# Kernel tuning notes

Hardware: AMD Instinct MI355X
Metric: run time of the kernel (lower is better)

Reference implementation:

```python
import jax, jax.numpy as jnp
import numpy as np

D_MODEL = 2048
HEADS = 16
K = D_MODEL // HEADS  # 128
FFN = 8192


def rms_norm(x):
    # mean of squares over last dim, no eps (matches source)
    ms = jnp.mean(jnp.square(x), axis=2, keepdims=True)
    return x / jnp.sqrt(ms)


def setup_inputs() -> dict:
    key = jax.random.key(0)
    ks = jax.random.split(key, 9)
    s = D_MODEL ** (-0.5)
    B, S = 2, 2048
    return {
        "x_BSE": jax.random.normal(ks[0], (B, S, D_MODEL), jnp.float32),
        "w_q": jax.random.normal(ks[1], (D_MODEL, HEADS, K), jnp.float32) * s,
        "w_k": jax.random.normal(ks[2], (D_MODEL, HEADS, K), jnp.float32) * s,
        "w_v": jax.random.normal(ks[3], (D_MODEL, HEADS, K), jnp.float32) * s,
        "w_o": jax.random.normal(ks[4], (D_MODEL, HEADS, K), jnp.float32) * s,
        "w1": jax.random.normal(ks[5], (D_MODEL, FFN), jnp.float32) * s,
        "b1": jax.random.normal(ks[6], (1, FFN), jnp.float32) * s,
        "w2": jax.random.normal(ks[7], (FFN, D_MODEL), jnp.float32) * s,
        "b2": jax.random.normal(ks[8], (1, D_MODEL), jnp.float32) * s,
    }


def attention(x, w_q, w_k, w_v, w_o):
    q = jnp.einsum('bse,ehk->bshk', x, w_q)
    k = jnp.einsum('bme,ehk->bmhk', x, w_k)
    v = jnp.einsum('bme,ehk->bmhk', x, w_v)
    logits = jnp.einsum('bshk,bmhk->bshm', q, k) / jnp.sqrt(jnp.float32(K))
    S = x.shape[1]
    causal = jnp.arange(S)[:, None] >= jnp.arange(S)[None, :]  # [S, M]
    logits = jnp.where(causal[None, :, None, :], logits, -jnp.inf)
    probs = jax.nn.softmax(logits, axis=3)
    out = jnp.einsum('bshm,bmhk->bshk', probs, v)
    return jnp.einsum('bshk,ehk->bse', out, w_o)


def ffn(x, w1, b1, w2, b2):
    h = jnp.clip(x @ w1 + b1, 0.0, 6.0)  # ReLU6
    return h @ w2 + b2


def reference(x_BSE, w_q, w_k, w_v, w_o, w1, b1, w2, b2):
    x = x_BSE + attention(rms_norm(x_BSE), w_q, w_k, w_v, w_o)
    x = x + ffn(rms_norm(x), w1, b1, w2, b2)
    return x
```

## Files before the change

### kernel.cpp

```cpp
#include <hip/hip_runtime.h>
#include <hip/hip_bf16.h>
#include <stdint.h>

typedef __attribute__((ext_vector_type(8))) short bf16x8;
typedef __attribute__((ext_vector_type(4))) float f32x4;
typedef unsigned short ushort_t;

typedef __attribute__((address_space(1))) char as1_char;
typedef __attribute__((address_space(3))) char as3_char;

__device__ __forceinline__ void gload_lds16(const void* g, void* l) {
  __builtin_amdgcn_global_load_lds((as1_char*)g, (as3_char*)l, 16, 0, 0);
}

template <int N> __device__ __forceinline__ void waitvm() {
  asm volatile("s_waitcnt vmcnt(%0)" :: "n"(N) : "memory");
}

__device__ __forceinline__ unsigned short f2bf(float f) {
  union { float f; unsigned u; } c; c.f = f;
  unsigned u = c.u;
  return (unsigned short)((u + 0x7fffu + ((u >> 16) & 1u)) >> 16);
}

__global__ __launch_bounds__(256)
void rmsnorm_kernel(const float* __restrict__ x, unsigned short* __restrict__ out) {
  const int tok = blockIdx.x;
  const int tid = threadIdx.x;
  const float4* xr = (const float4*)(x + (size_t)tok * 2048);
  float4 a = xr[tid];
  float4 b = xr[tid + 256];
  float s = a.x*a.x + a.y*a.y + a.z*a.z + a.w*a.w
          + b.x*b.x + b.y*b.y + b.z*b.z + b.w*b.w;
  #pragma unroll
  for (int m = 1; m < 64; m <<= 1) s += __shfl_xor(s, m);
  __shared__ float ws4[4];
  if ((tid & 63) == 0) ws4[tid >> 6] = s;
  __syncthreads();
  const float tot = ws4[0] + ws4[1] + ws4[2] + ws4[3];
  const float r = rsqrtf(tot * (1.0f / 2048.0f));
  ushort4 o1, o2;
  o1.x = f2bf(a.x * r); o1.y = f2bf(a.y * r); o1.z = f2bf(a.z * r); o1.w = f2bf(a.w * r);
  o2.x = f2bf(b.x * r); o2.y = f2bf(b.y * r); o2.z = f2bf(b.z * r); o2.w = f2bf(b.w * r);
  ushort4* orow = (ushort4*)(out + (size_t)tok * 2048);
  orow[tid] = o1;
  orow[tid + 256] = o2;
}

__global__ __launch_bounds__(256)
void transpose_cvt(const float* __restrict__ in, unsigned short* __restrict__ out,
                   int R, int C) {
  __shared__ float t[32][33];
  const int c0 = blockIdx.x * 32, r0 = blockIdx.y * 32;
  const int tx = threadIdx.x, ty = threadIdx.y;
  #pragma unroll
  for (int i = 0; i < 4; i++)
    t[ty + 8 * i][tx] = in[(size_t)(r0 + ty + 8 * i) * C + (c0 + tx)];
  __syncthreads();
  #pragma unroll
  for (int i = 0; i < 4; i++)
    out[(size_t)(c0 + ty + 8 * i) * R + (r0 + tx)] = f2bf(t[tx][ty + 8 * i]);
}

__global__ __launch_bounds__(256)
void cvt_bf16_kernel(const float* __restrict__ in, unsigned short* __restrict__ out, int n4) {
  const int i = blockIdx.x * 256 + threadIdx.x;
  if (i < n4) {
    float4 v = ((const float4*)in)[i];
    ushort4 o; o.x = f2bf(v.x); o.y = f2bf(v.y); o.z = f2bf(v.z); o.w = f2bf(v.w);
    ((ushort4*)out)[i] = o;
  }
}

template <int BN, int EPI>
__global__ __launch_bounds__(512, 2)
void gemm256(const ushort_t* __restrict__ A, const ushort_t* __restrict__ B,
             int K, int N,
             ushort_t* ob0, ushort_t* ob1, ushort_t* ob2, float* outf,
             const float* __restrict__ res, const float* __restrict__ bias,
             int nbx) {
  constexpr int LB = (BN * 64) / 8192;
  constexpr int LPT = 2 + LB;
  constexpr int NR = BN / 64;
  constexpr int WN = BN / 4;
  constexpr int BUFSZ = 16384 + BN * 64;
  __shared__ __align__(16) char smem[4 * BUFSZ];

  const int tid = threadIdx.x;
  const int lane = tid & 63;
  const int wid = tid >> 6;
  const int wm = wid >> 2, wn = wid & 3;
  const int ln15 = lane & 15, g = lane >> 4;

  int wg = blockIdx.x;
  const int cpx = gridDim.x >> 3;
  wg = (wg & 7) * cpx + (wg >> 3);
  const int bx = wg % nbx, by = wg / nbx;
  const int m0 = by * 256, n0 = bx * BN;

  const char* Ab = (const char*)(A + (size_t)m0 * K);
  const char* Bb = (const char*)(B + (size_t)n0 * K);
  const size_t rowb = (size_t)K * 2;
  const int NT = K >> 5;

  auto stage = [&](int t, int s) {
    char* As = smem + s * BUFSZ;
    char* Bs = As + 16384;
    const size_t kb = (size_t)t * 64;
    #pragma unroll
    for (int i = 0; i < 2; i++) {
      const int o = i * 8192 + tid * 16;
      const int row = o >> 6, col = o & 63;
      gload_lds16(Ab + (size_t)row * rowb + kb + (col ^ ((row & 3) << 4)), As + o);
    }
    #pragma unroll
    for (int i = 0; i < LB; i++) {
      const int o = i * 8192 + tid * 16;
      const int row = o >> 6, col = o & 63;
      gload_lds16(Bb + (size_t)row * rowb + kb + (col ^ ((row & 3) << 4)), Bs + o);
    }
  };

  f32x4 acc[8][NR] = {};

  stage(0, 0); stage(1, 1); stage(2, 2);

  for (int t = 0; t < NT; ++t) {
    if (t + 3 < NT) {
      stage(t + 3, (t + 3) & 3);
      waitvm<3 * LPT>();
    } else {
      const int rem = NT - 1 - t;
      if (rem >= 2)      waitvm<2 * LPT>();
      else if (rem == 1) waitvm<LPT>();
      else               waitvm<0>();
    }
    __builtin_amdgcn_s_barrier();

    const char* As = smem + (t & 3) * BUFSZ;
    const char* Bs = As + 16384;

    bf16x8 af[8], bfm[NR];
    #pragma unroll
    for (int mi = 0; mi < 8; mi++) {
      const int row = wm * 128 + mi * 16 + ln15;
      af[mi] = *(const bf16x8*)(As + row * 64 + ((g * 16) ^ ((row & 3) << 4)));
    }
    #pragma unroll
    for (int ni = 0; ni < NR; ni++) {
      const int row = wn * WN + ni * 16 + ln15;
      bfm[ni] = *(const bf16x8*)(Bs + row * 64 + ((g * 16) ^ ((row & 3) << 4)));
    }
    asm volatile("" ::: "memory");
    __builtin_amdgcn_s_barrier();

    __builtin_amdgcn_s_setprio(1);
    #pragma unroll
    for (int mi = 0; mi < 8; mi++)
      #pragma unroll
      for (int ni = 0; ni < NR; ni++)
        acc[mi][ni] = __builtin_amdgcn_mfma_f32_16x16x32_bf16(af[mi], bfm[ni], acc[mi][ni], 0, 0, 0);
    __builtin_amdgcn_s_setprio(0);
  }

  #pragma unroll
  for (int mi = 0; mi < 8; mi++) {
    const int mrow = m0 + wm * 128 + mi * 16 + g * 4;
    #pragma unroll
    for (int ni = 0; ni < NR; ni++) {
      const int ncol = n0 + wn * WN + ni * 16 + ln15;
      if (EPI == 0) {
        const int region = n0 >> 11;
        if (region == 0) {
          #pragma unroll
          for (int r = 0; r < 4; r++)
            ob0[(size_t)(mrow + r) * 2048 + ncol] = f2bf(acc[mi][ni][r]);
        } else if (region == 1) {
          #pragma unroll
          for (int r = 0; r < 4; r++)
            ob1[(size_t)(mrow + r) * 2048 + (ncol - 2048)] = f2bf(acc[mi][ni][r]);
        } else {
          const int bb = mrow >> 11, ss = mrow & 2047;
          const int ncv = ncol - 4096;
          const int hh = ncv >> 7, dd = ncv & 127;
          ushort4 v;
          v.x = f2bf(acc[mi][ni][0]); v.y = f2bf(acc[mi][ni][1]);
          v.z = f2bf(acc[mi][ni][2]); v.w = f2bf(acc[mi][ni][3]);
          *(ushort4*)(ob2 + ((size_t)((bb * 16 + hh) * 128 + dd)) * 2048 + ss) = v;
        }
      } else if (EPI == 2) {
        const float bv = bias[ncol];
        #pragma unroll
        for (int r = 0; r < 4; r++) {
          float v = acc[mi][ni][r] + bv;
          v = fminf(fmaxf(v, 0.0f), 6.0f);
          ob0[(size_t)(mrow + r) * N + ncol] = f2bf(v);
        }
      } else {
        const float bv = bias ? bias[ncol] : 0.0f;
        #pragma unroll
        for (int r = 0; r < 4; r++) {
          const size_t idx = (size_t)(mrow + r) * N + ncol;
          outf[idx] = res[idx] + acc[mi][ni][r] + bv;
        }
      }
    }
  }
}

__global__ __launch_bounds__(256)
void attn_kernel(const unsigned short* __restrict__ Qg,
                 const unsigned short* __restrict__ Kg,
                 const unsigned short* __restrict__ Vg,
                 unsigned short* __restrict__ Og) {
  __shared__ __align__(16) char smem[65536];
  const int tid = threadIdx.x, lane = tid & 63, wid = tid >> 6;
  const int g = lane >> 4, qq = lane & 15;
  const int pairx = blockIdx.x, h = blockIdx.y, b = blockIdx.z;

  auto stage = [&](int kv0, char* kdst, char* vdst) {
    #pragma unroll
    for (int i = 0; i < 4; i++) {
      const int oo = i * 4096 + tid * 16;
      const int rK = oo >> 8;
      const int sK = (oo & 255) ^ ((rK & 7) << 4);
      gload_lds16((const char*)Kg + ((size_t)(b * 2048 + kv0 + rK) * 2048 + h * 128) * 2 + sK,
                  kdst + oo);
      const int rV = oo >> 7;
      const int sV = (oo & 127) ^ ((rV & 7) << 4);
      gload_lds16((const char*)Vg + ((size_t)((b * 16 + h) * 128 + rV) * 2048 + kv0) * 2 + sV,
                  vdst + oo);
    }
  };

  for (int half = 0; half < 2; ++half) {
    const int qb = half ? (31 - pairx) : pairx;
    const int q0 = qb * 64;
    const int myq = q0 + wid * 16 + qq;
    const int nt = qb + 1;

    bf16x8 qf[4];
    const unsigned short* qp = Qg + ((size_t)(b * 2048 + myq)) * 2048 + h * 128 + g * 8;
    #pragma unroll
    for (int ks = 0; ks < 4; ks++) qf[ks] = *(const bf16x8*)(qp + ks * 32);

    stage(0, smem, smem + 16384);

    float m_run = -1e30f, l_run = 0.0f;
    f32x4 oacc[8] = {};

    for (int t = 0; t < nt; ++t) {
      const int cur = t & 1;
      char* kbc = cur ? smem + 32768 : smem;
      char* vbc = cur ? smem + 49152 : smem + 16384;
      char* kbn = cur ? smem : smem + 32768;
      char* vbn = cur ? smem + 16384 : smem + 49152;

      if (t + 1 < nt) {
        stage((t + 1) * 64, kbn, vbn);
        asm volatile("s_waitcnt vmcnt(8)" ::: "memory");
      } else {
        asm volatile("s_waitcnt vmcnt(0)" ::: "memory");
      }
      __builtin_amdgcn_s_barrier();
      asm volatile("" ::: "memory");

      const int kv0 = t * 64;

      f32x4 st[4] = {};
      __builtin_amdgcn_s_setprio(1);
      #pragma unroll
      for (int ks = 0; ks < 4; ks++) {
        #pragma unroll
        for (int f = 0; f < 4; f++) {
          const int row = f * 16 + qq;
          const int cb = ks * 64 + g * 16;
          bf16x8 kf = *(const bf16x8*)(kbc + row * 256 + (cb ^ ((row & 7) << 4)));
          st[f] = __builtin_amdgcn_mfma_f32_16x16x32_bf16(kf, qf[ks], st[f], 0, 0, 0);
        }
      }
      __builtin_amdgcn_s_setprio(0);

      float p[4][4];
      float tmax = -3.0e38f;
      const bool diag = (t == qb);
      #pragma unroll
      for (int f = 0; f < 4; f++) {
        #pragma unroll
        for (int r = 0; r < 4; r++) {
          float v = st[f][r] * 0.08838834764831845f;
          if (diag) {
            const int kv = kv0 + f * 16 + g * 4 + r;
            if (kv > myq) v = -3.0e38f;
          }
          p[f][r] = v;
          tmax = fmaxf(tmax, v);
        }
      }
      tmax = fmaxf(tmax, __shfl_xor(tmax, 16));
      tmax = fmaxf(tmax, __shfl_xor(tmax, 32));
      const float m_new = fmaxf(m_run, tmax);
      const float sf = __expf(m_run - m_new);
      m_run = m_new;
      float tsum = 0.0f;
      #pragma unroll
      for (int f = 0; f < 4; f++) {
        #pragma unroll
        for (int r = 0; r < 4; r++) {
          p[f][r] = __expf(p[f][r] - m_new);
          tsum += p[f][r];
        }
      }
      tsum += __shfl_xor(tsum, 16);
      tsum += __shfl_xor(tsum, 32);
      l_run = l_run * sf + tsum;

      unsigned pk[4][2];
      #pragma unroll
      for (int f = 0; f < 4; f++) {
        pk[f][0] = (unsigned)f2bf(p[f][0]) | ((unsigned)f2bf(p[f][1]) << 16);
        pk[f][1] = (unsigned)f2bf(p[f][2]) | ((unsigned)f2bf(p[f][3]) << 16);
      }
      bf16x8 pa[2];
      const int sel = g >> 1;
      #pragma unroll
      for (int ks2 = 0; ks2 < 2; ks2++) {
        unsigned d[4];
        #pragma unroll
        for (int u = 0; u < 2; u++) {
          const int sl = qq + (((2 * g + u) & 3) << 4);
          const unsigned lo0 = (unsigned)__shfl((int)pk[2 * ks2][0], sl);
          const unsigned hi0 = (unsigned)__shfl((int)pk[2 * ks2 + 1][0], sl);
          const unsigned lo1 = (unsigned)__shfl((int)pk[2 * ks2][1], sl);
          const unsigned hi1 = (unsigned)__shfl((int)pk[2 * ks2 + 1][1], sl);
          d[2 * u]     = sel ? hi0 : lo0;
          d[2 * u + 1] = sel ? hi1 : lo1;
        }
        union { unsigned u[4]; bf16x8 v; } cv;
        cv.u[0] = d[0]; cv.u[1] = d[1]; cv.u[2] = d[2]; cv.u[3] = d[3];
        pa[ks2] = cv.v;
      }

      float sfr[4];
      #pragma unroll
      for (int r = 0; r < 4; r++) sfr[r] = __shfl(sf, g * 4 + r);
      #pragma unroll
      for (int nf = 0; nf < 8; nf++) {
        oacc[nf][0] *= sfr[0]; oacc[nf][1] *= sfr[1];
        oacc[nf][2] *= sfr[2]; oacc[nf][3] *= sfr[3];
      }
      __builtin_amdgcn_s_setprio(1);
      #pragma unroll
      for (int nf = 0; nf < 8; nf++) {
        #pragma unroll
        for (int ks2 = 0; ks2 < 2; ks2++) {
          const int row = nf * 16 + qq;
          const int cb = ks2 * 64 + g * 16;
          bf16x8 vf = *(const bf16x8*)(vbc + row * 128 + (cb ^ ((row & 7) << 4)));
          oacc[nf] = __builtin_amdgcn_mfma_f32_16x16x32_bf16(pa[ks2], vf, oacc[nf], 0, 0, 0);
        }
      }
      __builtin_amdgcn_s_setprio(0);

      asm volatile("" ::: "memory");
      __builtin_amdgcn_s_barrier();
    }

    asm volatile("" ::: "memory");
    const float inv = 1.0f / l_run;
    float invr[4];
    #pragma unroll
    for (int r = 0; r < 4; r++) invr[r] = __shfl(inv, g * 4 + r);

    float* Osm = (float*)smem;
    #pragma unroll
    for (int nf = 0; nf < 8; nf++) {
      #pragma unroll
      for (int r = 0; r < 4; r++)
        Osm[(wid * 16 + g * 4 + r) * 132 + nf * 16 + qq] = oacc[nf][r] * invr[r];
    }
    __syncthreads();
    #pragma unroll
    for (int it = 0; it < 4; it++) {
      const int row = it * 16 + (tid >> 4);
      const int c0 = (tid & 15) * 8;
      const float* src = &Osm[row * 132 + c0];
      uint4 w;
      w.x = (unsigned)f2bf(src[0]) | ((unsigned)f2bf(src[1]) << 16);
      w.y = (unsigned)f2bf(src[2]) | ((unsigned)f2bf(src[3]) << 16);
      w.z = (unsigned)f2bf(src[4]) | ((unsigned)f2bf(src[5]) << 16);
      w.w = (unsigned)f2bf(src[6]) | ((unsigned)f2bf(src[7]) << 16);
      *(uint4*)(Og + (size_t)(b * 2048 + q0 + row) * 2048 + h * 128 + c0) = w;
    }
    __syncthreads();
  }
}

extern "C" void kernel_launch(void* const* d_in, const int* in_sizes, int n_in,
                              void* d_out, int out_size, void* d_ws, size_t ws_size,
                              hipStream_t stream) {
  (void)in_sizes; (void)n_in; (void)out_size; (void)ws_size;
  const float* x  = (const float*)d_in[0];
  const float* wq = (const float*)d_in[1];
  const float* wk = (const float*)d_in[2];
  const float* wv = (const float*)d_in[3];
  const float* wo = (const float*)d_in[4];
  const float* w1 = (const float*)d_in[5];
  const float* b1 = (const float*)d_in[6];
  const float* w2 = (const float*)d_in[7];
  const float* b2 = (const float*)d_in[8];
  float* out = (float*)d_out;
  char* ws = (char*)d_ws;

  ushort_t* wqkvT = (ushort_t*)(ws + 0);
  ushort_t* wqT = wqkvT;
  ushort_t* wkT = (ushort_t*)(ws + 8388608);
  ushort_t* wvT = (ushort_t*)(ws + 16777216);
  ushort_t* woC = (ushort_t*)(ws + 25165824);
  ushort_t* w1T = (ushort_t*)(ws + 33554432);
  ushort_t* w2T = (ushort_t*)(ws + 67108864);
  ushort_t* h1  = (ushort_t*)(ws + 100663296);
  ushort_t* Qb  = (ushort_t*)(ws + 117440512);
  ushort_t* Kb  = (ushort_t*)(ws + 134217728);
  ushort_t* Vt  = (ushort_t*)(ws + 150994944);
  ushort_t* hid = h1;
  ushort_t* att = (ushort_t*)(ws + 167772160);
  ushort_t* h2  = att;

  const dim3 tb(32, 8);
  transpose_cvt<<<dim3(64, 64), tb, 0, stream>>>(wq, wqT, 2048, 2048);
  transpose_cvt<<<dim3(64, 64), tb, 0, stream>>>(wk, wkT, 2048, 2048);
  transpose_cvt<<<dim3(64, 64), tb, 0, stream>>>(wv, wvT, 2048, 2048);
  cvt_bf16_kernel<<<4096, 256, 0, stream>>>(wo, woC, 1048576);
  transpose_cvt<<<dim3(256, 64), tb, 0, stream>>>(w1, w1T, 2048, 8192);
  transpose_cvt<<<dim3(64, 256), tb, 0, stream>>>(w2, w2T, 8192, 2048);

  rmsnorm_kernel<<<4096, 256, 0, stream>>>(x, h1);
  gemm256<256, 0><<<24 * 16, 512, 0, stream>>>(h1, wqkvT, 2048, 6144,
                                               Qb, Kb, Vt, nullptr, nullptr, nullptr, 24);
  attn_kernel<<<dim3(16, 16, 2), 256, 0, stream>>>(Qb, Kb, Vt, att);
  gemm256<128, 3><<<16 * 16, 512, 0, stream>>>(att, woC, 2048, 2048,
                                               nullptr, nullptr, nullptr, out, x, nullptr, 16);
  rmsnorm_kernel<<<4096, 256, 0, stream>>>(out, h2);
  gemm256<256, 2><<<32 * 16, 512, 0, stream>>>(h2, w1T, 2048, 8192,
                                               hid, nullptr, nullptr, nullptr, nullptr, b1, 32);
  gemm256<128, 3><<<16 * 16, 512, 0, stream>>>(hid, w2T, 8192, 2048,
                                               nullptr, nullptr, nullptr, out, out, b2, 16);
}
```

Baseline: 666.2 us.

## Restructure GEMM into 256x128 tiles with K=64 steps and triple-buffered split prefetch

Replaces the templated 256xBN GEMM with a fixed 256x128 tile kernel using 8 waves in a 4x2 layout. Each step now covers 64 of K with three LDS slots, and prefetch of stage t+2 is split into two halves interleaved with two MFMA phases, separated by extra barriers. It uses a wider 8-row XOR swizzle and launch bounds of one block per CU. The QKV and FFN1 GEMMs get more, smaller blocks. The aim is better load/compute overlap and fewer barriers per unit of K, at the cost of lower occupancy and lower per-block data reuse on the wide GEMMs.

```diff
diff --git a/kernel.cpp b/kernel.cpp
--- a/kernel.cpp
+++ b/kernel.cpp
@@ -72,103 +72,123 @@
   }
 }
 
-template <int BN, int EPI>
-__global__ __launch_bounds__(512, 2)
-void gemm256(const ushort_t* __restrict__ A, const ushort_t* __restrict__ B,
+template <int EPI>
+__global__ __launch_bounds__(512, 1)
+void gemm_r3(const ushort_t* __restrict__ A, const ushort_t* __restrict__ B,
              int K, int N,
              ushort_t* ob0, ushort_t* ob1, ushort_t* ob2, float* outf,
              const float* __restrict__ res, const float* __restrict__ bias,
              int nbx) {
-  constexpr int LB = (BN * 64) / 8192;
-  constexpr int LPT = 2 + LB;
-  constexpr int NR = BN / 64;
-  constexpr int WN = BN / 4;
-  constexpr int BUFSZ = 16384 + BN * 64;
-  __shared__ __align__(16) char smem[4 * BUFSZ];
+  constexpr int SLOT = 49152;
+  __shared__ __align__(16) char smem[3 * SLOT];
 
   const int tid = threadIdx.x;
   const int lane = tid & 63;
   const int wid = tid >> 6;
-  const int wm = wid >> 2, wn = wid & 3;
+  const int wm = wid >> 1, wn = wid & 1;
   const int ln15 = lane & 15, g = lane >> 4;
 
   int wg = blockIdx.x;
   const int cpx = gridDim.x >> 3;
   wg = (wg & 7) * cpx + (wg >> 3);
   const int bx = wg % nbx, by = wg / nbx;
-  const int m0 = by * 256, n0 = bx * BN;
+  const int m0 = by * 256, n0 = bx * 128;
 
   const char* Ab = (const char*)(A + (size_t)m0 * K);
   const char* Bb = (const char*)(B + (size_t)n0 * K);
   const size_t rowb = (size_t)K * 2;
-  const int NT = K >> 5;
-
-  auto stage = [&](int t, int s) {
-    char* As = smem + s * BUFSZ;
-    char* Bs = As + 16384;
-    const size_t kb = (size_t)t * 64;
+  const int NT = K >> 6;
+
+  auto stage_part = [&](int t, int slot, int part) {
+    char* As = smem + slot * SLOT;
+    char* Bs = As + 32768;
+    const size_t kb = (size_t)t * 128;
     #pragma unroll
     for (int i = 0; i < 2; i++) {
-      const int o = i * 8192 + tid * 16;
-      const int row = o >> 6, col = o & 63;
-      gload_lds16(Ab + (size_t)row * rowb + kb + (col ^ ((row & 3) << 4)), As + o);
-    }
-    #pragma unroll
-    for (int i = 0; i < LB; i++) {
-      const int o = i * 8192 + tid * 16;
-      const int row = o >> 6, col = o & 63;
-      gload_lds16(Bb + (size_t)row * rowb + kb + (col ^ ((row & 3) << 4)), Bs + o);
+      const int o = (part * 2 + i) * 8192 + tid * 16;
+      const int row = o >> 7, col = o & 127;
+      gload_lds16(Ab + (size_t)row * rowb + kb + (col ^ ((row & 7) << 4)), As + o);
+    }
+    {
+      const int o = part * 8192 + tid * 16;
+      const int row = o >> 7, col = o & 127;
+      gload_lds16(Bb + (size_t)row * rowb + kb + (col ^ ((row & 7) << 4)), Bs + o);
     }
   };
 
-  f32x4 acc[8][NR] = {};
-
-  stage(0, 0); stage(1, 1); stage(2, 2);
-
+  f32x4 acc[4][4] = {};
+
+  stage_part(0, 0, 0); stage_part(0, 0, 1);
+  if (NT > 1) { stage_part(1, 1, 0); stage_part(1, 1, 1); }
+
+  int slot = 0;
   for (int t = 0; t < NT; ++t) {
-    if (t + 3 < NT) {
-      stage(t + 3, (t + 3) & 3);
-      waitvm<3 * LPT>();
-    } else {
-      const int rem = NT - 1 - t;
-      if (rem >= 2)      waitvm<2 * LPT>();
-      else if (rem == 1) waitvm<LPT>();
-      else               waitvm<0>();
-    }
+    if (t + 1 < NT) waitvm<6>(); else waitvm<0>();
     __builtin_amdgcn_s_barrier();
 
-    const char* As = smem + (t & 3) * BUFSZ;
-    const char* Bs = As + 16384;
-
-    bf16x8 af[8], bfm[NR];
-    #pragma unroll
-    for (int mi = 0; mi < 8; mi++) {
-      const int row = wm * 128 + mi * 16 + ln15;
-      af[mi] = *(const bf16x8*)(As + row * 64 + ((g * 16) ^ ((row & 3) << 4)));
-    }
-    #pragma unroll
-    for (int ni = 0; ni < NR; ni++) {
-      const int row = wn * WN + ni * 16 + ln15;
-      bfm[ni] = *(const bf16x8*)(Bs + row * 64 + ((g * 16) ^ ((row & 3) << 4)));
-    }
-    asm volatile("" ::: "memory");
+    const char* As = smem + slot * SLOT;
+    const char* Bs = As + 32768;
+    const int slot2 = (slot + 2 >= 3) ? slot - 1 : slot + 2;
+    const bool pf = (t + 2 < NT);
+
+    bf16x8 bfm[4][2], af[2][2];
+    #pragma unroll
+    for (int ni = 0; ni < 4; ni++) {
+      const int row = wn * 64 + ni * 16 + ln15;
+      #pragma unroll
+      for (int kk = 0; kk < 2; kk++)
+        bfm[ni][kk] = *(const bf16x8*)(Bs + row * 128 + ((kk * 64 + g * 16) ^ ((row & 7) << 4)));
+    }
+    #pragma unroll
+    for (int mi = 0; mi < 2; mi++) {
+      const int row = wm * 64 + mi * 16 + ln15;
+      #pragma unroll
+      for (int kk = 0; kk < 2; kk++)
+        af[mi][kk] = *(const bf16x8*)(As + row * 128 + ((kk * 64 + g * 16) ^ ((row & 7) << 4)));
+    }
+    if (pf) stage_part(t + 2, slot2, 0);
     __builtin_amdgcn_s_barrier();
-
     __builtin_amdgcn_s_setprio(1);
     #pragma unroll
-    for (int mi = 0; mi < 8; mi++)
-      #pragma unroll
-      for (int ni = 0; ni < NR; ni++)
-        acc[mi][ni] = __builtin_amdgcn_mfma_f32_16x16x32_bf16(af[mi], bfm[ni], acc[mi][ni], 0, 0, 0);
+    for (int mi = 0; mi < 2; mi++)
+      #pragma unroll
+      for (int ni = 0; ni < 4; ni++)
+        #pragma unroll
+        for (int kk = 0; kk < 2; kk++)
+          acc[mi][ni] = __builtin_amdgcn_mfma_f32_16x16x32_bf16(af[mi][kk], bfm[ni][kk], acc[mi][ni], 0, 0, 0);
     __builtin_amdgcn_s_setprio(0);
+    __builtin_amdgcn_s_barrier();
+
+    bf16x8 af1[2][2];
+    #pragma unroll
+    for (int mi = 0; mi < 2; mi++) {
+      const int row = wm * 64 + (mi + 2) * 16 + ln15;
+      #pragma unroll
+      for (int kk = 0; kk < 2; kk++)
+        af1[mi][kk] = *(const bf16x8*)(As + row * 128 + ((kk * 64 + g * 16) ^ ((row & 7) << 4)));
+    }
+    if (pf) stage_part(t + 2, slot2, 1);
+    __builtin_amdgcn_s_barrier();
+    __builtin_amdgcn_s_setprio(1);
+    #pragma unroll
+    for (int mi = 0; mi < 2; mi++)
+      #pragma unroll
+      for (int ni = 0; ni < 4; ni++)
+        #pragma unroll
+        for (int kk = 0; kk < 2; kk++)
+          acc[mi + 2][ni] = __builtin_amdgcn_mfma_f32_16x16x32_bf16(af1[mi][kk], bfm[ni][kk], acc[mi + 2][ni], 0, 0, 0);
+    __builtin_amdgcn_s_setprio(0);
+    __builtin_amdgcn_s_barrier();
+
+    slot = (slot + 1 >= 3) ? 0 : slot + 1;
   }
 
   #pragma unroll
-  for (int mi = 0; mi < 8; mi++) {
-    const int mrow = m0 + wm * 128 + mi * 16 + g * 4;
-    #pragma unroll
-    for (int ni = 0; ni < NR; ni++) {
-      const int ncol = n0 + wn * WN + ni * 16 + ln15;
+  for (int mi = 0; mi < 4; mi++) {
+    const int mrow = m0 + wm * 64 + mi * 16 + g * 4;
+    #pragma unroll
+    for (int ni = 0; ni < 4; ni++) {
+      const int ncol = n0 + wn * 64 + ni * 16 + ln15;
       if (EPI == 0) {
         const int region = n0 >> 11;
         if (region == 0) {
@@ -436,14 +456,14 @@
   transpose_cvt<<<dim3(64, 256), tb, 0, stream>>>(w2, w2T, 8192, 2048);
 
   rmsnorm_kernel<<<4096, 256, 0, stream>>>(x, h1);
-  gemm256<256, 0><<<24 * 16, 512, 0, stream>>>(h1, wqkvT, 2048, 6144,
-                                               Qb, Kb, Vt, nullptr, nullptr, nullptr, 24);
+  gemm_r3<0><<<48 * 16, 512, 0, stream>>>(h1, wqkvT, 2048, 6144,
+                                          Qb, Kb, Vt, nullptr, nullptr, nullptr, 48);
   attn_kernel<<<dim3(16, 16, 2), 256, 0, stream>>>(Qb, Kb, Vt, att);
-  gemm256<128, 3><<<16 * 16, 512, 0, stream>>>(att, woC, 2048, 2048,
-                                               nullptr, nullptr, nullptr, out, x, nullptr, 16);
+  gemm_r3<3><<<16 * 16, 512, 0, stream>>>(att, woC, 2048, 2048,
+                                          nullptr, nullptr, nullptr, out, x, nullptr, 16);
   rmsnorm_kernel<<<4096, 256, 0, stream>>>(out, h2);
-  gemm256<256, 2><<<32 * 16, 512, 0, stream>>>(h2, w1T, 2048, 8192,
-                                               hid, nullptr, nullptr, nullptr, nullptr, b1, 32);
-  gemm256<128, 3><<<16 * 16, 512, 0, stream>>>(hid, w2T, 8192, 2048,
-                                               nullptr, nullptr, nullptr, out, out, b2, 16);
-}
+  gemm_r3<2><<<64 * 16, 512, 0, stream>>>(h2, w1T, 2048, 8192,
+                                          hid, nullptr, nullptr, nullptr, nullptr, b1, 64);
+  gemm_r3<3><<<16 * 16, 512, 0, stream>>>(hid, w2T, 8192, 2048,
+                                          nullptr, nullptr, nullptr, out, out, b2, 16);
+}
```

Result: faster. 618.6 us (-7.1%).
